# Kernel tuning notes

Hardware: AMD Instinct MI355X
Metric: run time of the kernel (lower is better)

The kernel has to match this reference:

```python
import jax, jax.numpy as jnp
import numpy as np

EPS = 1e-5
OFFSET_SCALE = 1.0
KPTS = 9   # 3x3 deformable kernel
GROUP = 1  # in_dim // out_dim


def _bn(x, g, b, m, v):
    # eval-mode BatchNorm2d on (B,C,H,W)
    s = g / jnp.sqrt(v + EPS)
    return x * s[None, :, None, None] + (b - m * s)[None, :, None, None]


def _dcnv4_core(value, offset, mask, offset_scale):
    # value: (B,H,W,G,Cg); offset: (B,H,W,G,K,2) as (dx,dy); mask: (B,H,W,G,K)
    B, H, W, G, Cg = value.shape
    K = mask.shape[-1]
    dt = value.dtype
    ky = jnp.repeat(jnp.arange(3) - 1, 3).astype(dt)
    kx = jnp.tile(jnp.arange(3) - 1, 3).astype(dt)
    grid = jnp.stack([kx, ky], -1)                                   # (K,2)
    base = jnp.stack(jnp.meshgrid(jnp.arange(W, dtype=dt),
                                  jnp.arange(H, dtype=dt),
                                  indexing='xy'), -1)                # (H,W,2) = (x,y)
    loc = base[None, :, :, None, None, :] + (grid + offset) * offset_scale  # (B,H,W,G,K,2)
    px, py = loc[..., 0], loc[..., 1]
    x0 = jnp.floor(px); y0 = jnp.floor(py)
    fx = px - x0; fy = py - y0
    vflat = value.transpose(0, 3, 1, 2, 4).reshape(B, G, H * W, Cg)
    out = jnp.zeros((B, G, H * W, Cg), dt)
    corners = ((0.0, 0.0, (1 - fx) * (1 - fy)), (1.0, 0.0, fx * (1 - fy)),
               (0.0, 1.0, (1 - fx) * fy), (1.0, 1.0, fx * fy))
    for dx, dy, wgt in corners:
        xi = x0 + dx; yi = y0 + dy
        valid = ((xi >= 0) & (xi < W) & (yi >= 0) & (yi < H)).astype(dt)
        idx = (jnp.clip(yi, 0, W and H - 1) * W + jnp.clip(xi, 0, W - 1)).astype(jnp.int32)
        idx = idx.transpose(0, 3, 1, 2, 4).reshape(B, G, H * W * K)
        v = jnp.take_along_axis(vflat, idx[..., None], axis=2).reshape(B, G, H * W, K, Cg)
        w = (wgt * valid * mask).transpose(0, 3, 1, 2, 4).reshape(B, G, H * W, K)
        out = out + jnp.einsum('bgsk,bgskc->bgsc', w, v)
    return out.reshape(B, G, H, W, Cg).transpose(0, 2, 3, 1, 4).reshape(B, H, W, G * Cg)


def setup_inputs() -> dict:
    key = jax.random.key(0)
    B, C, H, W = 8, 128, 64, 64
    C_OUT = 128
    OM = ((GROUP * KPTS * 3 + 7) // 8) * 8  # 32, offset_mask padded width
    ks = jax.random.split(key, 16)
    f = jnp.float32
    sc = 1.0 / np.sqrt(C).astype(np.float32)
    return {
        'x': jax.random.normal(ks[0], (B, C, H, W), f),
        'bn1_g': jax.random.uniform(ks[1], (C,), f, 0.5, 1.5),
        'bn1_b': jax.random.normal(ks[2], (C,), f) * 0.1,
        'bn1_m': jax.random.normal(ks[3], (C,), f) * 0.1,
        'bn1_v': jax.random.uniform(ks[4], (C,), f, 0.5, 1.5),
        'w_pw0': jax.random.normal(ks[5], (C, C), f) * sc,
        'w_vp': jax.random.normal(ks[6], (C, C), f) * sc,
        'b_vp': jnp.zeros((C,), f),
        'w_om': jax.random.normal(ks[7], (C, OM), f) * 0.01,
        'b_om': jnp.zeros((OM,), f),
        'w_op': jax.random.normal(ks[8], (C, C), f) * sc,
        'bn2_g': jax.random.uniform(ks[9], (C,), f, 0.5, 1.5),
        'bn2_b': jax.random.normal(ks[10], (C,), f) * 0.1,
        'bn2_m': jax.random.normal(ks[11], (C,), f) * 0.1,
        'bn2_v': jax.random.uniform(ks[12], (C,), f, 0.5, 1.5),
        'w_pw1': jax.random.normal(ks[13], (C_OUT, C), f) * sc,
    }


def reference(x, bn1_g, bn1_b, bn1_m, bn1_v, w_pw0, w_vp, b_vp, w_om, b_om, w_op,
              bn2_g, bn2_b, bn2_m, bn2_v, w_pw1):
    x = _bn(x, bn1_g, bn1_b, bn1_m, bn1_v)
    x = jnp.einsum('bchw,oc->bohw', x, w_pw0)
    B, C, H, W = x.shape
    x = x.reshape(B, H * W, C)  # raw reshape (faithful to torch .reshape, NOT a permute)
    G, K = GROUP, KPTS
    Cg = C // G
    value = (x @ w_vp + b_vp).reshape(B, H, W, G, Cg)
    om = (x @ w_om + b_om)[..., :G * K * 3].reshape(B, H, W, G, K, 3)
    out = _dcnv4_core(value, om[..., :2], om[..., 2], OFFSET_SCALE)
    out = out.reshape(B, H * W, C) @ w_op
    x = out.reshape(B, C, H, W)  # raw reshape back
    x = _bn(x, bn2_g, bn2_b, bn2_m, bn2_v)
    x = jnp.einsum('bchw,oc->bohw', x, w_pw1)
    return x
```

## Files before the change

kernel.cpp:

```cpp
#include <hip/hip_runtime.h>

#define HW 4096
#define PADF 33
#define PADU 136
typedef unsigned short ushort;
typedef __attribute__((ext_vector_type(8))) short short8;
typedef __attribute__((ext_vector_type(4))) float f32x4;

__device__ __forceinline__ ushort bf_rne(float f) {
  unsigned u = __float_as_uint(f);
  unsigned r = (u + 0x7fffu + ((u >> 16) & 1u)) >> 16;
  return (ushort)r;
}
__device__ __forceinline__ void split2(float f, ushort& hi, ushort& lo) {
  ushort h = bf_rne(f);
  float hf = __uint_as_float((unsigned)h << 16);
  hi = h;
  lo = bf_rne(f - hf);
}

__global__ __launch_bounds__(256) void prep(
    const float* __restrict__ g1, const float* __restrict__ be1,
    const float* __restrict__ m1, const float* __restrict__ v1,
    const float* __restrict__ w0,
    const float* __restrict__ g2, const float* __restrict__ be2,
    const float* __restrict__ m2, const float* __restrict__ v2,
    const float* __restrict__ w1,
    const float* __restrict__ wvp, const float* __restrict__ wom,
    const float* __restrict__ wop,
    ushort* __restrict__ W0h, ushort* __restrict__ W0l, float* __restrict__ b0,
    ushort* __restrict__ W1h, ushort* __restrict__ W1l, float* __restrict__ b1,
    ushort* __restrict__ vph, ushort* __restrict__ vpl,
    ushort* __restrict__ oph, ushort* __restrict__ opl,
    ushort* __restrict__ omh, ushort* __restrict__ oml)
{
  const int t = threadIdx.x;
  const int role = blockIdx.x;
  if (role < 16) {
    __shared__ float sc[128], sh[128], part[16][17];
    const int cv = role >> 3;
    const float* g  = cv ? g2 : g1;
    const float* be = cv ? be2 : be1;
    const float* mm = cv ? m2 : m1;
    const float* vv = cv ? v2 : v1;
    if (t < 128) {
      float s = g[t] / sqrtf(vv[t] + 1e-5f);
      sc[t] = s;
      sh[t] = be[t] - mm[t] * s;
    }
    __syncthreads();
    const float* ws = cv ? w1 : w0;
    ushort* dh = cv ? W1h : W0h;
    ushort* dl = cv ? W1l : W0l;
    float* bb  = cv ? b1 : b0;
    const int o = ((role & 7) << 4) + (t >> 4);
    const int kl = t & 15;
    float accb = 0.f;
    #pragma unroll
    for (int j = 0; j < 8; ++j) {
      const int k = (kl << 3) + j;
      const float wv = ws[o * 128 + k];
      ushort hi, lo;
      split2(wv * sc[k], hi, lo);
      dh[o * 128 + k] = hi;
      dl[o * 128 + k] = lo;
      accb = fmaf(wv, sh[k], accb);
    }
    part[t >> 4][kl] = accb;
    __syncthreads();
    if (kl == 0) {
      float s = 0.f;
      #pragma unroll
      for (int j = 0; j < 16; ++j) s += part[t >> 4][j];
      bb[o] = s;
    }
  } else if (role < 32) {
    const int rr = role & 7;
    const float* srcM = (role < 24) ? wvp : wop;
    ushort* dh = (role < 24) ? vph : oph;
    ushort* dl = (role < 24) ? vpl : opl;
    const int n = (rr << 4) + (t >> 4);
    const int kl = t & 15;
    #pragma unroll
    for (int j = 0; j < 8; ++j) {
      const int k = (kl << 3) + j;
      ushort hi, lo;
      split2(srcM[k * 128 + n], hi, lo);
      dh[n * 128 + k] = hi;
      dl[n * 128 + k] = lo;
    }
  } else {
    const int n = ((role - 32) << 4) + (t >> 4);
    const int kl = t & 15;
    #pragma unroll
    for (int j = 0; j < 8; ++j) {
      const int k = (kl << 3) + j;
      ushort hi, lo;
      split2(wom[k * 32 + n], hi, lo);
      omh[n * 128 + k] = hi;
      oml[n * 128 + k] = lo;
    }
  }
}

__global__ __launch_bounds__(512, 2) void fused_x_valom(
    const float* __restrict__ x,
    const ushort* __restrict__ W0h, const ushort* __restrict__ W0l,
    const float* __restrict__ b0,
    const ushort* __restrict__ vph, const ushort* __restrict__ vpl,
    const float* __restrict__ bvp, const float* __restrict__ bom,
    float* __restrict__ value, float* __restrict__ omb)
{
  __shared__ __align__(16) char smem[102912];
  __shared__ float b0_s[128], b2_s[160];
  ushort (*Wh_s)[32] = (ushort(*)[32])(smem);
  ushort (*Wl_s)[32] = (ushort(*)[32])(smem + 8192);
  float*  Xf         = (float*)(smem + 16384);
  ushort (*Vh_s)[32] = (ushort(*)[32])(smem);
  ushort (*Vl_s)[32] = (ushort(*)[32])(smem + 10240);
  ushort (*Yh)[PADU] = (ushort(*)[PADU])(smem + 33280);
  ushort (*Yl)[PADU] = (ushort(*)[PADU])(smem + 68096);

  const int t = threadIdx.x;
  const int cb = blockIdx.x;
  const int b = blockIdx.y;
  const int hwBase = cb << 7;
  const size_t xbase = (size_t)b * (size_t)(128 * HW);
  if (t < 128) b0_s[t] = b0[t];
  if (t < 160) b2_s[t] = (t < 128) ? bvp[t] : bom[t - 128];
  const int lane = t & 63, w = t >> 6;
  const int col = lane & 15, quad = lane >> 4;
  const f32x4 z = {0.f, 0.f, 0.f, 0.f};

  f32x4 acc1[8];
  #pragma unroll
  for (int f = 0; f < 8; ++f) acc1[f] = z;

  for (int kc = 0; kc < 4; ++kc) {
    const int kB = kc << 5;
    {
      const int o = t >> 2, q8 = (t & 3) << 3;
      *(uint4*)&Wh_s[o][q8] = *(const uint4*)&W0h[o * 128 + kB + q8];
      *(uint4*)&Wl_s[o][q8] = *(const uint4*)&W0l[o * 128 + kB + q8];
    }
    #pragma unroll
    for (int p = 0; p < 2; ++p) {
      const int idx = (p << 9) + t;
      const int c = idx >> 5, j4 = (idx & 31) << 2;
      const float4 f = *(const float4*)&x[xbase + (size_t)(kB + c) * HW + hwBase + j4];
      Xf[(j4 + 0) * PADF + c] = f.x;
      Xf[(j4 + 1) * PADF + c] = f.y;
      Xf[(j4 + 2) * PADF + c] = f.z;
      Xf[(j4 + 3) * PADF + c] = f.w;
    }
    __syncthreads();
    union { ushort u[8]; short8 v; } bh, bl;
    {
      const float* xr = &Xf[((w << 4) + col) * PADF + (quad << 3)];
      #pragma unroll
      for (int j = 0; j < 8; ++j) split2(xr[j], bh.u[j], bl.u[j]);
    }
    #pragma unroll
    for (int f = 0; f < 8; ++f) {
      const int row = (f << 4) + col;
      const short8 aH = *(const short8*)&Wh_s[row][quad << 3];
      const short8 aL = *(const short8*)&Wl_s[row][quad << 3];
      acc1[f] = __builtin_amdgcn_mfma_f32_16x16x32_bf16(aH, bh.v, acc1[f], 0, 0, 0);
      acc1[f] = __builtin_amdgcn_mfma_f32_16x16x32_bf16(aH, bl.v, acc1[f], 0, 0, 0);
      acc1[f] = __builtin_amdgcn_mfma_f32_16x16x32_bf16(aL, bh.v, acc1[f], 0, 0, 0);
    }
    __syncthreads();
  }

  #pragma unroll
  for (int f = 0; f < 8; ++f)
    #pragma unroll
    for (int r = 0; r < 4; ++r) {
      const int o = (f << 4) + (quad << 2) + r;
      const int j = (w << 4) + col;
      ushort hi, lo;
      split2(acc1[f][r] + b0_s[o], hi, lo);
      Yh[o][j] = hi;
      Yl[o][j] = lo;
    }

  const int wm2 = (w & 3) << 5;
  const int wn2 = (w >> 2) * 80;
  f32x4 acc2[2][5];
  #pragma unroll
  for (int i = 0; i < 2; ++i)
    #pragma unroll
    for (int j = 0; j < 5; ++j) acc2[i][j] = z;

  for (int j2 = 0; j2 < 4; ++j2) {
    for (int i = t; i < 640; i += 512) {
      const int n = i >> 2, q8 = (i & 3) << 3;
      *(uint4*)&Vh_s[n][q8] = *(const uint4*)&vph[n * 128 + (j2 << 5) + q8];
      *(uint4*)&Vl_s[n][q8] = *(const uint4*)&vpl[n * 128 + (j2 << 5) + q8];
    }
    __syncthreads();
    short8 aH[2], aL[2];
    #pragma unroll
    for (int f2 = 0; f2 < 2; ++f2) {
      const int row = wm2 + (f2 << 4) + col;
      aH[f2] = *(const short8*)&Yh[row][(j2 << 5) + (quad << 3)];
      aL[f2] = *(const short8*)&Yl[row][(j2 << 5) + (quad << 3)];
    }
    #pragma unroll
    for (int g2 = 0; g2 < 5; ++g2) {
      const int n = wn2 + (g2 << 4) + col;
      const short8 vh = *(const short8*)&Vh_s[n][quad << 3];
      const short8 vl = *(const short8*)&Vl_s[n][quad << 3];
      #pragma unroll
      for (int f2 = 0; f2 < 2; ++f2) {
        acc2[f2][g2] = __builtin_amdgcn_mfma_f32_16x16x32_bf16(aH[f2], vh, acc2[f2][g2], 0, 0, 0);
        acc2[f2][g2] = __builtin_amdgcn_mfma_f32_16x16x32_bf16(aH[f2], vl, acc2[f2][g2], 0, 0, 0);
        acc2[f2][g2] = __builtin_amdgcn_mfma_f32_16x16x32_bf16(aL[f2], vh, acc2[f2][g2], 0, 0, 0);
      }
    }
    __syncthreads();
  }
  #pragma unroll
  for (int f2 = 0; f2 < 2; ++f2)
    #pragma unroll
    for (int r = 0; r < 4; ++r) {
      const int m = wm2 + (f2 << 4) + (quad << 2) + r;
      const size_t gRow = (size_t)b * HW + (size_t)m * 32 + cb;
      #pragma unroll
      for (int g2 = 0; g2 < 5; ++g2) {
        const int n = wn2 + (g2 << 4) + col;
        const float v = acc2[f2][g2][r] + b2_s[n];
        if (n < 128) value[gRow * 128 + n] = v;
        else         omb[gRow * 32 + (n - 128)] = v;
      }
    }
}

__global__ __launch_bounds__(512, 2) void fused_sample_op_out(
    const float* __restrict__ value, const float* __restrict__ omb,
    const ushort* __restrict__ oph, const ushort* __restrict__ opl,
    const ushort* __restrict__ W1h, const ushort* __restrict__ W1l,
    const float* __restrict__ b1, float* __restrict__ out)
{
  __shared__ __align__(16) char smem[147456];
  __shared__ float b1_s[128];
  ushort (*Afh)[128][32]  = (ushort(*)[128][32])(smem);
  ushort (*Afl)[128][32]  = (ushort(*)[128][32])(smem + 32768);
  ushort (*Bh)[128][32]   = (ushort(*)[128][32])(smem + 65536);
  ushort (*Bl)[128][32]   = (ushort(*)[128][32])(smem + 98304);
  float  (*oms)[32]       = (float(*)[32])(smem + 131072);
  ushort (*Yh)[PADU]      = (ushort(*)[PADU])(smem);
  ushort (*Yl)[PADU]      = (ushort(*)[PADU])(smem + 34816);
  ushort (*W1h_)[128][32] = (ushort(*)[128][32])(smem + 69632);
  ushort (*W1l_)[128][32] = (ushort(*)[128][32])(smem + 102400);

  const int t = threadIdx.x;
  const int blk = blockIdx.x;
  const int b = blk & 7;
  const int cb = blk >> 3;
  if (t < 128) b1_s[t] = b1[t];
  const int lane = t & 63, w = t >> 6;
  const int col = lane & 15, quad = lane >> 4;
  const f32x4 z = {0.f, 0.f, 0.f, 0.f};

  {
    const int m0 = t >> 2, j8 = (t & 3) << 3;
    const size_t orow = ((size_t)b * HW + m0 * 32 + cb) * 32;
    *(float4*)&oms[m0][j8]     = *(const float4*)&omb[orow + j8];
    *(float4*)&oms[m0][j8 + 4] = *(const float4*)&omb[orow + j8 + 4];
  }
  #pragma unroll
  for (int i = 0; i < 4; ++i) {
    const int idx = (i << 9) + t;
    const int kc = idx >> 9, n = (idx >> 2) & 127, q8 = (idx & 3) << 3;
    *(uint4*)&Bh[kc][n][q8] = *(const uint4*)&oph[n * 128 + (kc << 5) + q8];
    *(uint4*)&Bl[kc][n][q8] = *(const uint4*)&opl[n * 128 + (kc << 5) + q8];
  }
  __syncthreads();

  {
    const int xhalf = lane >> 5;
    const int c4 = (lane & 31) << 2;
    const float* vb = value + (size_t)b * (size_t)(HW * 128) + c4;
    const int kcw = (lane & 31) >> 3;
    const int cow = (lane & 7) << 2;
    #pragma unroll 1
    for (int tt = 0; tt < 16; ++tt) {
      const int m = (w << 4) + tt;
      const int s = m * 32 + cb;
      const float fw = (float)(s & 63), fh = (float)(s >> 6);
      const float* omp = oms[m];
      float a0 = 0.f, a1 = 0.f, a2 = 0.f, a3 = 0.f;
      #pragma unroll
      for (int k = 0; k < 9; ++k) {
        const float dx = omp[k * 3 + 0];
        const float dy = omp[k * 3 + 1];
        const float mw = omp[k * 3 + 2];
        const float px = fw + (float)(k % 3 - 1) + dx;
        const float py = fh + (float)(k / 3 - 1) + dy;
        const float x0f = floorf(px), y0f = floorf(py);
        const float fx = px - x0f, fy = py - y0f;
        const int ix = (int)x0f + xhalf;
        const int iy = (int)y0f;
        const float wxm = (xhalf ? fx : 1.f - fx) * mw *
                          ((ix >= 0 && ix < 64) ? 1.f : 0.f);
        const int xc = min(max(ix, 0), 63);
        const int yc0 = min(max(iy, 0), 63);
        const int yc1 = min(max(iy + 1, 0), 63);
        const float w0 = wxm * (1.f - fy) * ((iy >= 0 && iy < 64) ? 1.f : 0.f);
        const float w1 = wxm * fy * ((iy + 1 >= 0 && iy + 1 < 64) ? 1.f : 0.f);
        const float4 v0 = *(const float4*)&vb[(size_t)((yc0 << 6) + xc) * 128];
        const float4 v1 = *(const float4*)&vb[(size_t)((yc1 << 6) + xc) * 128];
        a0 = fmaf(w0, v0.x, a0); a1 = fmaf(w0, v0.y, a1);
        a2 = fmaf(w0, v0.z, a2); a3 = fmaf(w0, v0.w, a3);
        a0 = fmaf(w1, v1.x, a0); a1 = fmaf(w1, v1.y, a1);
        a2 = fmaf(w1, v1.z, a2); a3 = fmaf(w1, v1.w, a3);
      }
      a0 += __shfl_xor(a0, 32); a1 += __shfl_xor(a1, 32);
      a2 += __shfl_xor(a2, 32); a3 += __shfl_xor(a3, 32);
      if (!xhalf) {
        ushort h0, l0, h1, l1, h2, l2, h3, l3;
        split2(a0, h0, l0); split2(a1, h1, l1);
        split2(a2, h2, l2); split2(a3, h3, l3);
        uint2 uh, ul;
        uh.x = (unsigned)h0 | ((unsigned)h1 << 16);
        uh.y = (unsigned)h2 | ((unsigned)h3 << 16);
        ul.x = (unsigned)l0 | ((unsigned)l1 << 16);
        ul.y = (unsigned)l2 | ((unsigned)l3 << 16);
        *(uint2*)&Afh[kcw][m][cow] = uh;
        *(uint2*)&Afl[kcw][m][cow] = ul;
      }
    }
  }
  __syncthreads();

  const int wm1 = (w & 1) << 6, wn1 = (w >> 1) << 5;
  f32x4 acc1[4][2];
  #pragma unroll
  for (int i = 0; i < 4; ++i) { acc1[i][0] = z; acc1[i][1] = z; }

  #pragma unroll 1
  for (int kc = 0; kc < 4; ++kc) {
    short8 aH[4], aL[4];
    #pragma unroll
    for (int f = 0; f < 4; ++f) {
      const int row = wm1 + (f << 4) + col;
      aH[f] = *(const short8*)&Afh[kc][row][quad << 3];
      aL[f] = *(const short8*)&Afl[kc][row][quad << 3];
    }
    #pragma unroll
    for (int g = 0; g < 2; ++g) {
      const int n = wn1 + (g << 4) + col;
      const short8 bh = *(const short8*)&Bh[kc][n][quad << 3];
      const short8 bl = *(const short8*)&Bl[kc][n][quad << 3];
      #pragma unroll
      for (int f = 0; f < 4; ++f) {
        acc1[f][g] = __builtin_amdgcn_mfma_f32_16x16x32_bf16(aH[f], bh, acc1[f][g], 0, 0, 0);
        acc1[f][g] = __builtin_amdgcn_mfma_f32_16x16x32_bf16(aH[f], bl, acc1[f][g], 0, 0, 0);
        acc1[f][g] = __builtin_amdgcn_mfma_f32_16x16x32_bf16(aL[f], bh, acc1[f][g], 0, 0, 0);
      }
    }
  }
  __syncthreads();

  #pragma unroll
  for (int i = 0; i < 4; ++i) {
    const int n = t >> 2, q8 = (t & 3) << 3;
    *(uint4*)&W1h_[i][n][q8] = *(const uint4*)&W1h[n * 128 + (i << 5) + q8];
    *(uint4*)&W1l_[i][n][q8] = *(const uint4*)&W1l[n * 128 + (i << 5) + q8];
  }
  #pragma unroll
  for (int f = 0; f < 4; ++f)
    #pragma unroll
    for (int g = 0; g < 2; ++g)
      #pragma unroll
      for (int r = 0; r < 4; ++r) {
        const int ch = wm1 + (f << 4) + (quad << 2) + r;
        const int j  = wn1 + (g << 4) + col;
        ushort hi, lo;
        split2(acc1[f][g][r], hi, lo);
        Yh[j][ch] = hi;
        Yl[j][ch] = lo;
      }
  __syncthreads();

  const int wm2 = (w & 1) << 6, wn2 = (w >> 1) << 5;
  f32x4 acc2[4][2];
  #pragma unroll
  for (int i = 0; i < 4; ++i) { acc2[i][0] = z; acc2[i][1] = z; }

  #pragma unroll 1
  for (int j2 = 0; j2 < 4; ++j2) {
    short8 aH[4], aL[4];
    #pragma unroll
    for (int f2 = 0; f2 < 4; ++f2) {
      const int row = wm2 + (f2 << 4) + col;
      aH[f2] = *(const short8*)&W1h_[j2][row][quad << 3];
      aL[f2] = *(const short8*)&W1l_[j2][row][quad << 3];
    }
    #pragma unroll
    for (int g2 = 0; g2 < 2; ++g2) {
      const int j = wn2 + (g2 << 4) + col;
      const short8 bh = *(const short8*)&Yh[j][(j2 << 5) + (quad << 3)];
      const short8 bl = *(const short8*)&Yl[j][(j2 << 5) + (quad << 3)];
      #pragma unroll
      for (int f2 = 0; f2 < 4; ++f2) {
        acc2[f2][g2] = __builtin_amdgcn_mfma_f32_16x16x32_bf16(aH[f2], bh, acc2[f2][g2], 0, 0, 0);
        acc2[f2][g2] = __builtin_amdgcn_mfma_f32_16x16x32_bf16(aH[f2], bl, acc2[f2][g2], 0, 0, 0);
        acc2[f2][g2] = __builtin_amdgcn_mfma_f32_16x16x32_bf16(aL[f2], bh, acc2[f2][g2], 0, 0, 0);
      }
    }
  }
  const size_t obase = (size_t)b * (size_t)(128 * HW) + ((size_t)cb << 7);
  #pragma unroll
  for (int f2 = 0; f2 < 4; ++f2)
    #pragma unroll
    for (int r = 0; r < 4; ++r) {
      const int o = wm2 + (f2 << 4) + (quad << 2) + r;
      #pragma unroll
      for (int g2 = 0; g2 < 2; ++g2) {
        const int j = wn2 + (g2 << 4) + col;
        out[obase + (size_t)o * HW + j] = acc2[f2][g2][r] + b1_s[o];
      }
    }
}

extern "C" void kernel_launch(void* const* d_in, const int* in_sizes, int n_in,
                              void* d_out, int out_size, void* d_ws, size_t ws_size,
                              hipStream_t stream)
{
  const float* x    = (const float*)d_in[0];
  const float* g1   = (const float*)d_in[1];
  const float* be1  = (const float*)d_in[2];
  const float* m1   = (const float*)d_in[3];
  const float* v1   = (const float*)d_in[4];
  const float* wpw0 = (const float*)d_in[5];
  const float* wvp  = (const float*)d_in[6];
  const float* bvp  = (const float*)d_in[7];
  const float* womW = (const float*)d_in[8];
  const float* bom  = (const float*)d_in[9];
  const float* wop  = (const float*)d_in[10];
  const float* g2   = (const float*)d_in[11];
  const float* be2  = (const float*)d_in[12];
  const float* m2   = (const float*)d_in[13];
  const float* v2   = (const float*)d_in[14];
  const float* wpw1 = (const float*)d_in[15];

  char* ws = (char*)d_ws;
  float*  value = (float*) (ws + 0);
  float*  omb   = (float*) (ws + 16777216);
  size_t o = 20971520;
  ushort* W0h = (ushort*)(ws + o); o += 32768;
  ushort* W0l = (ushort*)(ws + o); o += 32768;
  ushort* W1h = (ushort*)(ws + o); o += 32768;
  ushort* W1l = (ushort*)(ws + o); o += 32768;
  ushort* vph = (ushort*)(ws + o); o += 40960;
  ushort* vpl = (ushort*)(ws + o); o += 40960;
  ushort* oph = (ushort*)(ws + o); o += 32768;
  ushort* opl = (ushort*)(ws + o); o += 32768;
  float*  b0  = (float*)(ws + o);  o += 512;
  float*  b1  = (float*)(ws + o);
  ushort* omh = vph + 128 * 128;
  ushort* oml = vpl + 128 * 128;

  prep<<<34, 256, 0, stream>>>(g1, be1, m1, v1, wpw0, g2, be2, m2, v2, wpw1,
                               wvp, womW, wop,
                               W0h, W0l, b0, W1h, W1l, b1,
                               vph, vpl, oph, opl, omh, oml);
  fused_x_valom<<<dim3(32, 8), 512, 0, stream>>>(x, W0h, W0l, b0, vph, vpl,
                                                 bvp, bom, value, omb);
  fused_sample_op_out<<<dim3(256), 512, 0, stream>>>(value, omb, oph, opl,
                                                     W1h, W1l, b1, (float*)d_out);
}
```

Baseline: 148.1 us.

## Prefetch next weight/input chunks into registers and vectorize Y stores

Software-pipelines the global loads of W0, x, and the value/offset projection weights by loading the next K-chunk into registers right after the barrier, so global latency overlaps the MFMA work. W1 weights are prefetched into registers before the second kernel's first GEMM, the sampling loop is unrolled by two, and the transposed Y hi/lo stores are packed into 64-bit writes. This raises register pressure, which may lower occupancy.

```diff
diff --git a/kernel.cpp b/kernel.cpp
--- a/kernel.cpp
+++ b/kernel.cpp
@@ -132,28 +132,39 @@
   const int col = lane & 15, quad = lane >> 4;
   const f32x4 z = {0.f, 0.f, 0.f, 0.f};
 
+  const int oW = t >> 2, q8W = (t & 3) << 3;
+  const int c0i = t >> 5, j40i = (t & 31) << 2;
+  const int c1i = (512 + t) >> 5, j41i = ((512 + t) & 31) << 2;
+
   f32x4 acc1[8];
   #pragma unroll
   for (int f = 0; f < 8; ++f) acc1[f] = z;
 
+  uint4 wch = *(const uint4*)&W0h[oW * 128 + q8W];
+  uint4 wcl = *(const uint4*)&W0l[oW * 128 + q8W];
+  float4 xc0 = *(const float4*)&x[xbase + (size_t)c0i * HW + hwBase + j40i];
+  float4 xc1 = *(const float4*)&x[xbase + (size_t)c1i * HW + hwBase + j41i];
+
+  #pragma unroll
   for (int kc = 0; kc < 4; ++kc) {
-    const int kB = kc << 5;
-    {
-      const int o = t >> 2, q8 = (t & 3) << 3;
-      *(uint4*)&Wh_s[o][q8] = *(const uint4*)&W0h[o * 128 + kB + q8];
-      *(uint4*)&Wl_s[o][q8] = *(const uint4*)&W0l[o * 128 + kB + q8];
-    }
-    #pragma unroll
-    for (int p = 0; p < 2; ++p) {
-      const int idx = (p << 9) + t;
-      const int c = idx >> 5, j4 = (idx & 31) << 2;
-      const float4 f = *(const float4*)&x[xbase + (size_t)(kB + c) * HW + hwBase + j4];
-      Xf[(j4 + 0) * PADF + c] = f.x;
-      Xf[(j4 + 1) * PADF + c] = f.y;
-      Xf[(j4 + 2) * PADF + c] = f.z;
-      Xf[(j4 + 3) * PADF + c] = f.w;
-    }
+    *(uint4*)&Wh_s[oW][q8W] = wch;
+    *(uint4*)&Wl_s[oW][q8W] = wcl;
+    Xf[(j40i + 0) * PADF + c0i] = xc0.x;
+    Xf[(j40i + 1) * PADF + c0i] = xc0.y;
+    Xf[(j40i + 2) * PADF + c0i] = xc0.z;
+    Xf[(j40i + 3) * PADF + c0i] = xc0.w;
+    Xf[(j41i + 0) * PADF + c1i] = xc1.x;
+    Xf[(j41i + 1) * PADF + c1i] = xc1.y;
+    Xf[(j41i + 2) * PADF + c1i] = xc1.z;
+    Xf[(j41i + 3) * PADF + c1i] = xc1.w;
     __syncthreads();
+    if (kc < 3) {
+      const int kB = (kc + 1) << 5;
+      wch = *(const uint4*)&W0h[oW * 128 + kB + q8W];
+      wcl = *(const uint4*)&W0l[oW * 128 + kB + q8W];
+      xc0 = *(const float4*)&x[xbase + (size_t)(kB + c0i) * HW + hwBase + j40i];
+      xc1 = *(const float4*)&x[xbase + (size_t)(kB + c1i) * HW + hwBase + j41i];
+    }
     union { ushort u[8]; short8 v; } bh, bl;
     {
       const float* xr = &Xf[((w << 4) + col) * PADF + (quad << 3)];
@@ -172,6 +183,16 @@
     __syncthreads();
   }
 
+  const int nV0 = t >> 2, qV0 = (t & 3) << 3;
+  const int nV1 = (t + 512) >> 2, qV1 = ((t + 512) & 3) << 3;
+  uint4 vh0, vl0, vh1, vl1;
+  vh0 = *(const uint4*)&vph[nV0 * 128 + qV0];
+  vl0 = *(const uint4*)&vpl[nV0 * 128 + qV0];
+  if (t < 128) {
+    vh1 = *(const uint4*)&vph[nV1 * 128 + qV1];
+    vl1 = *(const uint4*)&vpl[nV1 * 128 + qV1];
+  }
+
   #pragma unroll
   for (int f = 0; f < 8; ++f)
     #pragma unroll
@@ -192,13 +213,24 @@
     #pragma unroll
     for (int j = 0; j < 5; ++j) acc2[i][j] = z;
 
+  #pragma unroll
   for (int j2 = 0; j2 < 4; ++j2) {
-    for (int i = t; i < 640; i += 512) {
-      const int n = i >> 2, q8 = (i & 3) << 3;
-      *(uint4*)&Vh_s[n][q8] = *(const uint4*)&vph[n * 128 + (j2 << 5) + q8];
-      *(uint4*)&Vl_s[n][q8] = *(const uint4*)&vpl[n * 128 + (j2 << 5) + q8];
+    *(uint4*)&Vh_s[nV0][qV0] = vh0;
+    *(uint4*)&Vl_s[nV0][qV0] = vl0;
+    if (t < 128) {
+      *(uint4*)&Vh_s[nV1][qV1] = vh1;
+      *(uint4*)&Vl_s[nV1][qV1] = vl1;
     }
     __syncthreads();
+    if (j2 < 3) {
+      const int kB = (j2 + 1) << 5;
+      vh0 = *(const uint4*)&vph[nV0 * 128 + kB + qV0];
+      vl0 = *(const uint4*)&vpl[nV0 * 128 + kB + qV0];
+      if (t < 128) {
+        vh1 = *(const uint4*)&vph[nV1 * 128 + kB + qV1];
+        vl1 = *(const uint4*)&vpl[nV1 * 128 + kB + qV1];
+      }
+    }
     short8 aH[2], aL[2];
     #pragma unroll
     for (int f2 = 0; f2 < 2; ++f2) {
@@ -284,7 +316,7 @@
     const float* vb = value + (size_t)b * (size_t)(HW * 128) + c4;
     const int kcw = (lane & 31) >> 3;
     const int cow = (lane & 7) << 2;
-    #pragma unroll 1
+    #pragma unroll 2
     for (int tt = 0; tt < 16; ++tt) {
       const int m = (w << 4) + tt;
       const int s = m * 32 + cb;
@@ -334,6 +366,14 @@
   }
   __syncthreads();
 
+  const int nW = t >> 2, q8W = (t & 3) << 3;
+  uint4 w1rH[4], w1rL[4];
+  #pragma unroll
+  for (int ii = 0; ii < 4; ++ii) {
+    w1rH[ii] = *(const uint4*)&W1h[nW * 128 + (ii << 5) + q8W];
+    w1rL[ii] = *(const uint4*)&W1l[nW * 128 + (ii << 5) + q8W];
+  }
+
   const int wm1 = (w & 1) << 6, wn1 = (w >> 1) << 5;
   f32x4 acc1[4][2];
   #pragma unroll
@@ -364,24 +404,27 @@
   __syncthreads();
 
   #pragma unroll
-  for (int i = 0; i < 4; ++i) {
-    const int n = t >> 2, q8 = (t & 3) << 3;
-    *(uint4*)&W1h_[i][n][q8] = *(const uint4*)&W1h[n * 128 + (i << 5) + q8];
-    *(uint4*)&W1l_[i][n][q8] = *(const uint4*)&W1l[n * 128 + (i << 5) + q8];
+  for (int ii = 0; ii < 4; ++ii) {
+    *(uint4*)&W1h_[ii][nW][q8W] = w1rH[ii];
+    *(uint4*)&W1l_[ii][nW][q8W] = w1rL[ii];
   }
   #pragma unroll
   for (int f = 0; f < 4; ++f)
     #pragma unroll
-    for (int g = 0; g < 2; ++g)
-      #pragma unroll
-      for (int r = 0; r < 4; ++r) {
-        const int ch = wm1 + (f << 4) + (quad << 2) + r;
-        const int j  = wn1 + (g << 4) + col;
-        ushort hi, lo;
-        split2(acc1[f][g][r], hi, lo);
-        Yh[j][ch] = hi;
-        Yl[j][ch] = lo;
-      }
+    for (int g = 0; g < 2; ++g) {
+      const int j   = wn1 + (g << 4) + col;
+      const int chb = wm1 + (f << 4) + (quad << 2);
+      ushort h0, l0, h1, l1, h2, l2, h3, l3;
+      split2(acc1[f][g][0], h0, l0); split2(acc1[f][g][1], h1, l1);
+      split2(acc1[f][g][2], h2, l2); split2(acc1[f][g][3], h3, l3);
+      uint2 uh, ul;
+      uh.x = (unsigned)h0 | ((unsigned)h1 << 16);
+      uh.y = (unsigned)h2 | ((unsigned)h3 << 16);
+      ul.x = (unsigned)l0 | ((unsigned)l1 << 16);
+      ul.y = (unsigned)l2 | ((unsigned)l3 << 16);
+      *(uint2*)&Yh[j][chb] = uh;
+      *(uint2*)&Yl[j][chb] = ul;
+    }
   __syncthreads();
 
   const int wm2 = (w & 1) << 6, wn2 = (w >> 1) << 5;
```

Measured after the change: 152.2 us. 1.03x slower.

## Precompute bilinear weights and indices in LDS, prefetch W1, vectorize Y stores

Applied to the files above, without the earlier changes.

Bilinear corner weights and clamped indices for each (pixel, kernel point) are now computed once cooperatively and stored in shared memory as compact records. Before, both x-halves of every wave recomputed them inside the sampling loop. The W1 weights are loaded into registers before the first MFMA stage so the global latency overlaps compute, and the Y hi/lo stores are packed into 8-byte writes. The costs are more LDS per block, which may affect the two-blocks-per-CU occupancy target, and extra register pressure from the prefetched W1 data.

```diff
diff --git a/kernel.cpp b/kernel.cpp
--- a/kernel.cpp
+++ b/kernel.cpp
@@ -236,19 +236,24 @@
     }
 }
 
+struct __align__(8) WgtRec {
+  float w00, w10, w01, w11;
+  ushort i00, i10, i01, i11;
+};
+
 __global__ __launch_bounds__(512, 2) void fused_sample_op_out(
     const float* __restrict__ value, const float* __restrict__ omb,
     const ushort* __restrict__ oph, const ushort* __restrict__ opl,
     const ushort* __restrict__ W1h, const ushort* __restrict__ W1l,
     const float* __restrict__ b1, float* __restrict__ out)
 {
-  __shared__ __align__(16) char smem[147456];
+  __shared__ __align__(16) char smem[158720];
   __shared__ float b1_s[128];
   ushort (*Afh)[128][32]  = (ushort(*)[128][32])(smem);
   ushort (*Afl)[128][32]  = (ushort(*)[128][32])(smem + 32768);
   ushort (*Bh)[128][32]   = (ushort(*)[128][32])(smem + 65536);
   ushort (*Bl)[128][32]   = (ushort(*)[128][32])(smem + 98304);
-  float  (*oms)[32]       = (float(*)[32])(smem + 131072);
+  WgtRec (*wgt)[9]        = (WgtRec(*)[9])(smem + 131072);
   ushort (*Yh)[PADU]      = (ushort(*)[PADU])(smem);
   ushort (*Yl)[PADU]      = (ushort(*)[PADU])(smem + 34816);
   ushort (*W1h_)[128][32] = (ushort(*)[128][32])(smem + 69632);
@@ -263,18 +268,41 @@
   const int col = lane & 15, quad = lane >> 4;
   const f32x4 z = {0.f, 0.f, 0.f, 0.f};
 
-  {
-    const int m0 = t >> 2, j8 = (t & 3) << 3;
-    const size_t orow = ((size_t)b * HW + m0 * 32 + cb) * 32;
-    *(float4*)&oms[m0][j8]     = *(const float4*)&omb[orow + j8];
-    *(float4*)&oms[m0][j8 + 4] = *(const float4*)&omb[orow + j8 + 4];
-  }
   #pragma unroll
   for (int i = 0; i < 4; ++i) {
     const int idx = (i << 9) + t;
     const int kc = idx >> 9, n = (idx >> 2) & 127, q8 = (idx & 3) << 3;
     *(uint4*)&Bh[kc][n][q8] = *(const uint4*)&oph[n * 128 + (kc << 5) + q8];
     *(uint4*)&Bl[kc][n][q8] = *(const uint4*)&opl[n * 128 + (kc << 5) + q8];
+  }
+  for (int p = t; p < 1152; p += 512) {
+    const int m = p / 9, k = p - m * 9;
+    const int s = m * 32 + cb;
+    const size_t ob = ((size_t)b * HW + s) * 32 + k * 3;
+    const float dx = omb[ob], dy = omb[ob + 1], mw = omb[ob + 2];
+    const float px = (float)(s & 63) + (float)(k % 3 - 1) + dx;
+    const float py = (float)(s >> 6) + (float)(k / 3 - 1) + dy;
+    const float x0f = floorf(px), y0f = floorf(py);
+    const float fx = px - x0f, fy = py - y0f;
+    const int ix = (int)x0f, iy = (int)y0f;
+    const float vx0 = (ix >= 0 && ix < 64) ? 1.f : 0.f;
+    const float vx1 = (ix >= -1 && ix < 63) ? 1.f : 0.f;
+    const float vy0 = (iy >= 0 && iy < 64) ? 1.f : 0.f;
+    const float vy1 = (iy >= -1 && iy < 63) ? 1.f : 0.f;
+    const int xc0 = min(max(ix, 0), 63), xc1 = min(max(ix + 1, 0), 63);
+    const int yc0 = min(max(iy, 0), 63), yc1 = min(max(iy + 1, 0), 63);
+    const float gx0 = (1.f - fx) * mw * vx0;
+    const float gx1 = fx * mw * vx1;
+    WgtRec r;
+    r.w00 = gx0 * (1.f - fy) * vy0;
+    r.w10 = gx1 * (1.f - fy) * vy0;
+    r.w01 = gx0 * fy * vy1;
+    r.w11 = gx1 * fy * vy1;
+    r.i00 = (ushort)((yc0 << 6) + xc0);
+    r.i10 = (ushort)((yc0 << 6) + xc1);
+    r.i01 = (ushort)((yc1 << 6) + xc0);
+    r.i11 = (ushort)((yc1 << 6) + xc1);
+    wgt[m][k] = r;
   }
   __syncthreads();
 
@@ -284,37 +312,23 @@
     const float* vb = value + (size_t)b * (size_t)(HW * 128) + c4;
     const int kcw = (lane & 31) >> 3;
     const int cow = (lane & 7) << 2;
-    #pragma unroll 1
+    #pragma unroll 2
     for (int tt = 0; tt < 16; ++tt) {
       const int m = (w << 4) + tt;
-      const int s = m * 32 + cb;
-      const float fw = (float)(s & 63), fh = (float)(s >> 6);
-      const float* omp = oms[m];
       float a0 = 0.f, a1 = 0.f, a2 = 0.f, a3 = 0.f;
       #pragma unroll
       for (int k = 0; k < 9; ++k) {
-        const float dx = omp[k * 3 + 0];
-        const float dy = omp[k * 3 + 1];
-        const float mw = omp[k * 3 + 2];
-        const float px = fw + (float)(k % 3 - 1) + dx;
-        const float py = fh + (float)(k / 3 - 1) + dy;
-        const float x0f = floorf(px), y0f = floorf(py);
-        const float fx = px - x0f, fy = py - y0f;
-        const int ix = (int)x0f + xhalf;
-        const int iy = (int)y0f;
-        const float wxm = (xhalf ? fx : 1.f - fx) * mw *
-                          ((ix >= 0 && ix < 64) ? 1.f : 0.f);
-        const int xc = min(max(ix, 0), 63);
-        const int yc0 = min(max(iy, 0), 63);
-        const int yc1 = min(max(iy + 1, 0), 63);
-        const float w0 = wxm * (1.f - fy) * ((iy >= 0 && iy < 64) ? 1.f : 0.f);
-        const float w1 = wxm * fy * ((iy + 1 >= 0 && iy + 1 < 64) ? 1.f : 0.f);
-        const float4 v0 = *(const float4*)&vb[(size_t)((yc0 << 6) + xc) * 128];
-        const float4 v1 = *(const float4*)&vb[(size_t)((yc1 << 6) + xc) * 128];
-        a0 = fmaf(w0, v0.x, a0); a1 = fmaf(w0, v0.y, a1);
-        a2 = fmaf(w0, v0.z, a2); a3 = fmaf(w0, v0.w, a3);
-        a0 = fmaf(w1, v1.x, a0); a1 = fmaf(w1, v1.y, a1);
-        a2 = fmaf(w1, v1.z, a2); a3 = fmaf(w1, v1.w, a3);
+        const WgtRec r = wgt[m][k];
+        const float wA = xhalf ? r.w10 : r.w00;
+        const float wB = xhalf ? r.w11 : r.w01;
+        const int iA = xhalf ? (int)r.i10 : (int)r.i00;
+        const int iB = xhalf ? (int)r.i11 : (int)r.i01;
+        const float4 v0 = *(const float4*)&vb[(size_t)iA * 128];
+        const float4 v1 = *(const float4*)&vb[(size_t)iB * 128];
+        a0 = fmaf(wA, v0.x, a0); a1 = fmaf(wA, v0.y, a1);
+        a2 = fmaf(wA, v0.z, a2); a3 = fmaf(wA, v0.w, a3);
+        a0 = fmaf(wB, v1.x, a0); a1 = fmaf(wB, v1.y, a1);
+        a2 = fmaf(wB, v1.z, a2); a3 = fmaf(wB, v1.w, a3);
       }
       a0 += __shfl_xor(a0, 32); a1 += __shfl_xor(a1, 32);
       a2 += __shfl_xor(a2, 32); a3 += __shfl_xor(a3, 32);
@@ -334,6 +348,14 @@
   }
   __syncthreads();
 
+  const int nW = t >> 2, q8W = (t & 3) << 3;
+  uint4 w1rH[4], w1rL[4];
+  #pragma unroll
+  for (int ii = 0; ii < 4; ++ii) {
+    w1rH[ii] = *(const uint4*)&W1h[nW * 128 + (ii << 5) + q8W];
+    w1rL[ii] = *(const uint4*)&W1l[nW * 128 + (ii << 5) + q8W];
+  }
+
   const int wm1 = (w & 1) << 6, wn1 = (w >> 1) << 5;
   f32x4 acc1[4][2];
   #pragma unroll
@@ -364,24 +386,27 @@
   __syncthreads();
 
   #pragma unroll
-  for (int i = 0; i < 4; ++i) {
-    const int n = t >> 2, q8 = (t & 3) << 3;
-    *(uint4*)&W1h_[i][n][q8] = *(const uint4*)&W1h[n * 128 + (i << 5) + q8];
-    *(uint4*)&W1l_[i][n][q8] = *(const uint4*)&W1l[n * 128 + (i << 5) + q8];
+  for (int ii = 0; ii < 4; ++ii) {
+    *(uint4*)&W1h_[ii][nW][q8W] = w1rH[ii];
+    *(uint4*)&W1l_[ii][nW][q8W] = w1rL[ii];
   }
   #pragma unroll
   for (int f = 0; f < 4; ++f)
     #pragma unroll
-    for (int g = 0; g < 2; ++g)
-      #pragma unroll
-      for (int r = 0; r < 4; ++r) {
-        const int ch = wm1 + (f << 4) + (quad << 2) + r;
-        const int j  = wn1 + (g << 4) + col;
-        ushort hi, lo;
-        split2(acc1[f][g][r], hi, lo);
-        Yh[j][ch] = hi;
-        Yl[j][ch] = lo;
-      }
+    for (int g = 0; g < 2; ++g) {
+      const int j   = wn1 + (g << 4) + col;
+      const int chb = wm1 + (f << 4) + (quad << 2);
+      ushort h0, l0, h1, l1, h2, l2, h3, l3;
+      split2(acc1[f][g][0], h0, l0); split2(acc1[f][g][1], h1, l1);
+      split2(acc1[f][g][2], h2, l2); split2(acc1[f][g][3], h3, l3);
+      uint2 uh, ul;
+      uh.x = (unsigned)h0 | ((unsigned)h1 << 16);
+      uh.y = (unsigned)h2 | ((unsigned)h3 << 16);
+      ul.x = (unsigned)l0 | ((unsigned)l1 << 16);
+      ul.y = (unsigned)l2 | ((unsigned)l3 << 16);
+      *(uint2*)&Yh[j][chb] = uh;
+      *(uint2*)&Yl[j][chb] = ul;
+    }
   __syncthreads();
 
   const int wm2 = (w & 1) << 6, wn2 = (w >> 1) << 5;
```

Measured after the change: 148.5 us. About the same (+0.3%).
